# Performance work log

Hardware: AMD Instinct MI355X
Metric: run time of the kernel (lower is better)

The kernel has to match this reference:

```python
import jax, jax.numpy as jnp
import numpy as np

N = 65536          # nodes
E = 1048576        # edges (avg degree 16)
K = 5              # B-spline kernel size per dim (dim=3 -> 125 kernels)
F_IN, F_OUT = 1, 32
GRID = 32          # first sparse_voxel_max_pool: size = 1/32 -> 32^3 voxels
NUM_VOX = GRID ** 3

# enumerate the 2^3 corners of the degree-1 B-spline support
_BITS = np.array([[(b >> d) & 1 for d in range(3)] for b in range(8)], dtype=np.int32)  # [8,3]
_STRIDES = np.array([1, K, K * K], dtype=np.int32)  # kernel index strides per dim


def setup_inputs() -> dict:
    key = jax.random.key(0)
    ks = jax.random.split(key, 7)
    x = jax.random.normal(ks[0], (N, F_IN), dtype=jnp.float32)
    edge_index = jax.random.randint(ks[1], (2, E), 0, N, dtype=jnp.int32)
    pseudo = jax.random.uniform(ks[2], (E, 3), dtype=jnp.float32)   # edge pseudo-coords in [0,1]^3
    pos = jax.random.uniform(ks[3], (N, 3), dtype=jnp.float32)      # node positions in [0,1]^3
    W = jax.random.normal(ks[4], (K ** 3, F_IN, F_OUT), dtype=jnp.float32) * 0.1
    W_root = jax.random.normal(ks[5], (F_IN, F_OUT), dtype=jnp.float32) * 0.1
    bias = jax.random.normal(ks[6], (F_OUT,), dtype=jnp.float32) * 0.1
    return {"x": x, "edge_index": edge_index, "pseudo": pseudo, "pos": pos,
            "W": W, "W_root": W_root, "bias": bias}


def spline_basis(pseudo):
    """Degree-1 open B-spline basis. Returns (weights [E,8], kernel_idx [E,8])."""
    v = pseudo * (K - 1)                                   # [E,3] in [0, K-1]
    i0 = jnp.clip(jnp.floor(v), 0, K - 2)                  # lower knot per dim
    f = v - i0                                             # fractional part
    i0 = i0.astype(jnp.int32)
    bits = jnp.asarray(_BITS)                              # [8,3]
    idx = i0[:, None, :] + bits[None]                      # [E,8,3]
    w = jnp.where(bits[None].astype(bool), f[:, None, :], 1.0 - f[:, None, :])
    B = w.prod(axis=-1)                                    # [E,8]
    kidx = (idx * jnp.asarray(_STRIDES)).sum(axis=-1)      # [E,8] in [0,125)
    return B, kidx


def spline_conv(x, edge_index, pseudo, W, W_root, bias):
    src, dst = edge_index[0], edge_index[1]
    B, kidx = spline_basis(pseudo)                         # [E,8], [E,8]
    xj = x[src]                                            # [E,F_IN] edge-wise gather
    Wg = W[kidx]                                           # [E,8,F_IN,F_OUT]
    msg = jnp.einsum('es,ef,esfo->eo', B, xj, Wg)          # basis-weighted messages [E,F_OUT]
    agg = jax.ops.segment_sum(msg, dst, num_segments=N)    # scatter-add
    deg = jax.ops.segment_sum(jnp.ones((E,), jnp.float32), dst, num_segments=N)
    out = agg / jnp.clip(deg, 1.0)[:, None] + x @ W_root + bias  # mean aggr + root + bias
    return out


def reference(x, edge_index, pseudo, pos, W, W_root, bias):
    h = jax.nn.elu(spline_conv(x, edge_index, pseudo, W, W_root, bias))  # [N,32]
    # sparse voxel max pooling: hash positions to a 32^3 grid, scatter-max features
    vid = jnp.clip(jnp.floor(pos * GRID), 0, GRID - 1).astype(jnp.int32)  # [N,3]
    vidx = vid[:, 0] + GRID * vid[:, 1] + GRID * GRID * vid[:, 2]         # [N]
    pooled = jax.ops.segment_max(h, vidx, num_segments=NUM_VOX)           # [32768,32]
    pooled = jnp.where(jnp.isfinite(pooled), pooled, 0.0)                 # empty voxels -> 0
    return pooled
```

## Files before the change

### kernel.cpp

```cpp
#include <hip/hip_runtime.h>
#include <math.h>

#define F_OUT     32
#define GRID_DIM  32
#define NUM_VOX   (GRID_DIM * GRID_DIM * GRID_DIM)

#define NGRP  256
#define GNPB  256
#define HNPB  128
#define SEB   2048
#define EPT   4
#define BCAP  4480
#define SCS   132
#define DEGS  125
#define CSTR  32

__device__ __forceinline__ unsigned int enc_f32(float f) {
    unsigned int u = __float_as_uint(f);
    return (u & 0x80000000u) ? ~u : (u | 0x80000000u);
}
__device__ __forceinline__ float dec_f32(unsigned int e) {
    return (e & 0x80000000u) ? __uint_as_float(e ^ 0x80000000u)
                             : __uint_as_float(~e);
}

__global__ __launch_bounds__(512) void scatter_kernel(
    const int*   __restrict__ src,
    const int*   __restrict__ dst,
    const float* __restrict__ x,
    const float* __restrict__ pseudo,
    float4* __restrict__ payload,
    unsigned int* __restrict__ cursor,
    int E)
{
    __shared__ unsigned int sHist[NGRP];
    __shared__ unsigned int sStart[NGRP];
    __shared__ unsigned int sGBase[NGRP];
    __shared__ unsigned int sTotal;
    __shared__ unsigned short sGid[SEB];
    __shared__ __align__(16) float4 sPay[SEB];

    const int t  = threadIdx.x;
    const int e0 = blockIdx.x * SEB;

    if (t < NGRP) sHist[t] = 0;
    __syncthreads();

    unsigned short dloc[EPT];
    float4 pay[EPT];
    bool   val[EPT];
    #pragma unroll
    for (int i = 0; i < EPT; ++i) {
        int e = e0 + i * 512 + t;
        val[i] = (e < E);
        if (val[i]) {
            int d = dst[e];
            int s = src[e];
            float p0 = pseudo[3 * e], p1 = pseudo[3 * e + 1], p2 = pseudo[3 * e + 2];
            float xj = x[s];
            unsigned int q2 = (unsigned int)(p2 * 65535.0f + 0.5f) & 0xFFFFu;
            pay[i]  = make_float4(p0, p1, xj,
                        __uint_as_float(q2 | ((unsigned int)(d & 255) << 16)));
            dloc[i] = (unsigned short)d;
            atomicAdd(&sHist[(d >> 8) & 255], 1u);
        } else dloc[i] = 0;
    }
    __syncthreads();

    if (t < 64) {
        unsigned int c0 = sHist[4*t], c1 = sHist[4*t+1], c2 = sHist[4*t+2], c3 = sHist[4*t+3];
        unsigned int loc = c0 + c1 + c2 + c3;
        unsigned int incl = loc;
        #pragma unroll
        for (int d = 1; d < 64; d <<= 1) {
            unsigned int v = __shfl_up(incl, d, 64);
            if (t >= d) incl += v;
        }
        unsigned int excl = incl - loc;
        sStart[4*t]   = excl;
        sStart[4*t+1] = excl + c0;
        sStart[4*t+2] = excl + c0 + c1;
        sStart[4*t+3] = excl + c0 + c1 + c2;
        if (t == 63) sTotal = incl;
    }
    __syncthreads();

    if (t < NGRP) {
        unsigned int c = sHist[t];
        sGBase[t] = c ? atomicAdd(&cursor[(size_t)t * CSTR], c) : 0u;
        sHist[t]  = sStart[t];
    }
    __syncthreads();

    #pragma unroll
    for (int i = 0; i < EPT; ++i) {
        if (val[i]) {
            unsigned int g = ((unsigned int)dloc[i] >> 8) & 255u;
            unsigned int slot = atomicAdd(&sHist[g], 1u);
            sPay[slot] = pay[i];
            sGid[slot] = (unsigned short)g;
        }
    }
    __syncthreads();

    const unsigned int total = sTotal;
    for (unsigned int i = t; i < total; i += 512) {
        unsigned int g   = sGid[i];
        unsigned int idx = sGBase[g] + (i - sStart[g]);
        if (idx < BCAP)
            payload[(size_t)g * BCAP + idx] = sPay[i];
    }
}

__device__ __forceinline__ void process_edge(float4 r, float* sC, int half)
{
    unsigned int w = __float_as_uint(r.w);
    int rel8 = (int)((w >> 16) & 255u);
    if ((rel8 >> 7) != half) return;

    float xj = r.z;
    float p2 = (float)(w & 0xFFFFu) * (1.0f / 65535.0f);

    float v0 = r.x * 4.0f, v1 = r.y * 4.0f, v2 = p2 * 4.0f;
    float i0 = fminf(fmaxf(floorf(v0), 0.0f), 3.0f);
    float i1 = fminf(fmaxf(floorf(v1), 0.0f), 3.0f);
    float i2 = fminf(fmaxf(floorf(v2), 0.0f), 3.0f);
    float f0 = v0 - i0, f1 = v1 - i1, f2 = v2 - i2;
    float g0 = 1.0f - f0, g1 = 1.0f - f1, g2 = 1.0f - f2;
    int k = (int)i0 + 5 * (int)i1 + 25 * (int)i2;

    float w00 = g0 * g1, w10 = f0 * g1, w01 = g0 * f1, w11 = f0 * f1;
    float a2 = xj * g2, b2 = xj * f2;
    float* row = sC + (rel8 & 127) * SCS;
    atomicAdd(row + k +  0, w00 * a2);
    atomicAdd(row + k +  1, w10 * a2);
    atomicAdd(row + k +  5, w01 * a2);
    atomicAdd(row + k +  6, w11 * a2);
    atomicAdd(row + k + 25, w00 * b2);
    atomicAdd(row + k + 26, w10 * b2);
    atomicAdd(row + k + 30, w01 * b2);
    atomicAdd(row + k + 31, w11 * b2);
    atomicAdd(row + DEGS, 1.0f);
}

__global__ __launch_bounds__(256) void owner_kernel(
    const float4* __restrict__ payload,
    const unsigned int* __restrict__ cursor,
    const float* __restrict__ W,
    const float* __restrict__ x,
    const float* __restrict__ W_root,
    const float* __restrict__ bias,
    const float* __restrict__ pos,
    unsigned int* __restrict__ pooled,
    int Nn)
{
    __shared__ __align__(16) float sC[HNPB * SCS];

    const int t    = threadIdx.x;
    const int g    = blockIdx.x >> 1;
    const int half = blockIdx.x & 1;

    for (int i = t; i < HNPB * SCS / 4; i += 256)
        ((float4*)sC)[i] = make_float4(0.f, 0.f, 0.f, 0.f);

    int cnt = (int)cursor[(size_t)g * CSTR];
    if (cnt > BCAP) cnt = BCAP;
    const float4* slab = payload + (size_t)g * BCAP;
    __syncthreads();

    {
        int i = t;
        if (i < cnt) {
            float4 r = slab[i];
            for (i += 256; i < cnt; i += 256) {
                float4 rn = slab[i];
                process_edge(r, sC, half);
                r = rn;
            }
            process_edge(r, sC, half);
        }
    }
    __syncthreads();

    const int nl = t & 31;
    const int cg = t >> 5;
    const float4 wr = *(const float4*)(W_root + cg * 4);
    const float4 bs = *(const float4*)(bias + cg * 4);

    #pragma unroll
    for (int tile = 0; tile < 4; ++tile) {
        const int node = tile * 32 + nl;
        const float* crow = sC + node * SCS;
        float4 acc = make_float4(0.f, 0.f, 0.f, 0.f);
        #pragma unroll 8
        for (int k4 = 0; k4 < 31; ++k4) {
            float4 r = *(const float4*)&crow[k4 * 4];
            const float* wp = W + (k4 * 4) * F_OUT + cg * 4;
            float4 w0 = *(const float4*)(wp);
            float4 w1 = *(const float4*)(wp + F_OUT);
            float4 w2 = *(const float4*)(wp + 2 * F_OUT);
            float4 w3 = *(const float4*)(wp + 3 * F_OUT);
            acc.x += r.x * w0.x + r.y * w1.x + r.z * w2.x + r.w * w3.x;
            acc.y += r.x * w0.y + r.y * w1.y + r.z * w2.y + r.w * w3.y;
            acc.z += r.x * w0.z + r.y * w1.z + r.z * w2.z + r.w * w3.z;
            acc.w += r.x * w0.w + r.y * w1.w + r.z * w2.w + r.w * w3.w;
        }
        {
            float r = crow[124];
            const float* wp = W + 124 * F_OUT + cg * 4;
            acc.x += r * wp[0]; acc.y += r * wp[1];
            acc.z += r * wp[2]; acc.w += r * wp[3];
        }
        float dg = fmaxf(crow[DEGS], 1.0f);
        int   n  = g * GNPB + half * HNPB + node;
        float xn = (n < Nn) ? x[n] : 0.0f;
        __syncthreads();
        if (n < Nn) {
            float h;
            h = acc.x / dg + xn * wr.x + bs.x; h = h > 0.f ? h : expm1f(h); sC[node * SCS + cg * 4 + 0] = h;
            h = acc.y / dg + xn * wr.y + bs.y; h = h > 0.f ? h : expm1f(h); sC[node * SCS + cg * 4 + 1] = h;
            h = acc.z / dg + xn * wr.z + bs.z; h = h > 0.f ? h : expm1f(h); sC[node * SCS + cg * 4 + 2] = h;
            h = acc.w / dg + xn * wr.w + bs.w; h = h > 0.f ? h : expm1f(h); sC[node * SCS + cg * 4 + 3] = h;
        }
    }
    __syncthreads();

    for (int item = t; item < HNPB * F_OUT; item += 256) {
        int nr = item >> 5, o = item & 31;
        int nn = g * GNPB + half * HNPB + nr;
        if (nn >= Nn) continue;
        int vx = min(max((int)floorf(pos[3 * nn + 0] * (float)GRID_DIM), 0), GRID_DIM - 1);
        int vy = min(max((int)floorf(pos[3 * nn + 1] * (float)GRID_DIM), 0), GRID_DIM - 1);
        int vz = min(max((int)floorf(pos[3 * nn + 2] * (float)GRID_DIM), 0), GRID_DIM - 1);
        int vidx = vx + GRID_DIM * vy + GRID_DIM * GRID_DIM * vz;
        atomicMax(&pooled[(size_t)vidx * F_OUT + o], enc_f32(sC[nr * SCS + o]));
    }
}

__global__ __launch_bounds__(256) void finalize_kernel(
    const unsigned int* pooled,
    float* out, int M)
{
    int i = blockIdx.x * blockDim.x + threadIdx.x;
    if (i >= M) return;
    unsigned int u = pooled[i];
    out[i] = (u == 0u) ? 0.0f : dec_f32(u);
}

extern "C" void kernel_launch(void* const* d_in, const int* in_sizes, int n_in,
                              void* d_out, int out_size, void* d_ws, size_t ws_size,
                              hipStream_t stream) {
    const float* x       = (const float*)d_in[0];
    const int*   ei      = (const int*)  d_in[1];
    const float* pseudo  = (const float*)d_in[2];
    const float* pos     = (const float*)d_in[3];
    const float* W       = (const float*)d_in[4];
    const float* W_root  = (const float*)d_in[5];
    const float* bias    = (const float*)d_in[6];

    const int E    = in_sizes[1] / 2;
    const int Nn   = in_sizes[0];
    const int nSB  = (E + SEB - 1) / SEB;
    const int nb   = 2 * ((Nn + GNPB - 1) / GNPB);

    float4*       payload = (float4*)d_ws;
    unsigned int* cursor  = (unsigned int*)((char*)d_ws + (size_t)NGRP * BCAP * sizeof(float4));

    unsigned int* pooled = (unsigned int*)d_out;
    const int M = (out_size < NUM_VOX * F_OUT) ? out_size : NUM_VOX * F_OUT;

    hipMemsetAsync(cursor, 0, (size_t)NGRP * CSTR * sizeof(unsigned int), stream);
    hipMemsetAsync(d_out, 0, (size_t)M * sizeof(float), stream);

    scatter_kernel<<<nSB, 512, 0, stream>>>(ei, ei + E, x, pseudo, payload, cursor, E);
    owner_kernel<<<nb, 256, 0, stream>>>(payload, cursor, W, x, W_root, bias, pos,
                                         pooled, Nn);
    finalize_kernel<<<(M + 255) / 256, 256, 0, stream>>>(pooled, (float*)d_out, M);
}
```

Before: 179.4 us.

## Bucket edges into 512 groups of 128 nodes so owner blocks read only their own edges

The scatter pass now buckets edges by destination into 512 groups of 128 nodes instead of 256 groups of 256. Each owner block handles one group with 512 threads and no longer skips the half of its slab that belongs to the other half-block. This removes the duplicated payload reads and rejection checks, since each edge is read once instead of twice. In exchange the scatter histogram grows and slab capacity per group shrinks to 2560, which risks overflow and silently dropped edges if a group gets more edges than the cap.

```diff
diff --git a/kernel.cpp b/kernel.cpp
--- a/kernel.cpp
+++ b/kernel.cpp
@@ -5,12 +5,11 @@
 #define GRID_DIM  32
 #define NUM_VOX   (GRID_DIM * GRID_DIM * GRID_DIM)
 
-#define NGRP  256
-#define GNPB  256
+#define NGRP  512
 #define HNPB  128
 #define SEB   2048
 #define EPT   4
-#define BCAP  4480
+#define BCAP  2560
 #define SCS   132
 #define DEGS  125
 #define CSTR  32
@@ -43,7 +42,7 @@
     const int t  = threadIdx.x;
     const int e0 = blockIdx.x * SEB;
 
-    if (t < NGRP) sHist[t] = 0;
+    sHist[t] = 0;
     __syncthreads();
 
     unsigned short dloc[EPT];
@@ -60,32 +59,31 @@
             float xj = x[s];
             unsigned int q2 = (unsigned int)(p2 * 65535.0f + 0.5f) & 0xFFFFu;
             pay[i]  = make_float4(p0, p1, xj,
-                        __uint_as_float(q2 | ((unsigned int)(d & 255) << 16)));
+                        __uint_as_float(q2 | ((unsigned int)(d & 127) << 16)));
             dloc[i] = (unsigned short)d;
-            atomicAdd(&sHist[(d >> 8) & 255], 1u);
+            atomicAdd(&sHist[(d >> 7) & (NGRP - 1)], 1u);
         } else dloc[i] = 0;
     }
     __syncthreads();
 
     if (t < 64) {
-        unsigned int c0 = sHist[4*t], c1 = sHist[4*t+1], c2 = sHist[4*t+2], c3 = sHist[4*t+3];
-        unsigned int loc = c0 + c1 + c2 + c3;
+        unsigned int c[8], loc = 0;
+        #pragma unroll
+        for (int j = 0; j < 8; ++j) { c[j] = sHist[8 * t + j]; loc += c[j]; }
         unsigned int incl = loc;
         #pragma unroll
         for (int d = 1; d < 64; d <<= 1) {
             unsigned int v = __shfl_up(incl, d, 64);
             if (t >= d) incl += v;
         }
-        unsigned int excl = incl - loc;
-        sStart[4*t]   = excl;
-        sStart[4*t+1] = excl + c0;
-        sStart[4*t+2] = excl + c0 + c1;
-        sStart[4*t+3] = excl + c0 + c1 + c2;
-        if (t == 63) sTotal = incl;
-    }
-    __syncthreads();
-
-    if (t < NGRP) {
+        unsigned int run = incl - loc;
+        #pragma unroll
+        for (int j = 0; j < 8; ++j) { sStart[8 * t + j] = run; run += c[j]; }
+        if (t == 63) sTotal = run;
+    }
+    __syncthreads();
+
+    {
         unsigned int c = sHist[t];
         sGBase[t] = c ? atomicAdd(&cursor[(size_t)t * CSTR], c) : 0u;
         sHist[t]  = sStart[t];
@@ -95,7 +93,7 @@
     #pragma unroll
     for (int i = 0; i < EPT; ++i) {
         if (val[i]) {
-            unsigned int g = ((unsigned int)dloc[i] >> 8) & 255u;
+            unsigned int g = ((unsigned int)dloc[i] >> 7) & (NGRP - 1);
             unsigned int slot = atomicAdd(&sHist[g], 1u);
             sPay[slot] = pay[i];
             sGid[slot] = (unsigned short)g;
@@ -112,11 +110,10 @@
     }
 }
 
-__device__ __forceinline__ void process_edge(float4 r, float* sC, int half)
+__device__ __forceinline__ void process_edge(float4 r, float* sC)
 {
     unsigned int w = __float_as_uint(r.w);
-    int rel8 = (int)((w >> 16) & 255u);
-    if ((rel8 >> 7) != half) return;
+    int rel = (int)((w >> 16) & 127u);
 
     float xj = r.z;
     float p2 = (float)(w & 0xFFFFu) * (1.0f / 65535.0f);
@@ -131,7 +128,7 @@
 
     float w00 = g0 * g1, w10 = f0 * g1, w01 = g0 * f1, w11 = f0 * f1;
     float a2 = xj * g2, b2 = xj * f2;
-    float* row = sC + (rel8 & 127) * SCS;
+    float* row = sC + rel * SCS;
     atomicAdd(row + k +  0, w00 * a2);
     atomicAdd(row + k +  1, w10 * a2);
     atomicAdd(row + k +  5, w01 * a2);
@@ -143,7 +140,7 @@
     atomicAdd(row + DEGS, 1.0f);
 }
 
-__global__ __launch_bounds__(256) void owner_kernel(
+__global__ __launch_bounds__(512) void owner_kernel(
     const float4* __restrict__ payload,
     const unsigned int* __restrict__ cursor,
     const float* __restrict__ W,
@@ -156,11 +153,10 @@
 {
     __shared__ __align__(16) float sC[HNPB * SCS];
 
-    const int t    = threadIdx.x;
-    const int g    = blockIdx.x >> 1;
-    const int half = blockIdx.x & 1;
-
-    for (int i = t; i < HNPB * SCS / 4; i += 256)
+    const int t = threadIdx.x;
+    const int g = blockIdx.x;
+
+    for (int i = t; i < HNPB * SCS / 4; i += 512)
         ((float4*)sC)[i] = make_float4(0.f, 0.f, 0.f, 0.f);
 
     int cnt = (int)cursor[(size_t)g * CSTR];
@@ -172,24 +168,24 @@
         int i = t;
         if (i < cnt) {
             float4 r = slab[i];
-            for (i += 256; i < cnt; i += 256) {
+            for (i += 512; i < cnt; i += 512) {
                 float4 rn = slab[i];
-                process_edge(r, sC, half);
+                process_edge(r, sC);
                 r = rn;
             }
-            process_edge(r, sC, half);
-        }
-    }
-    __syncthreads();
-
-    const int nl = t & 31;
-    const int cg = t >> 5;
+            process_edge(r, sC);
+        }
+    }
+    __syncthreads();
+
+    const int nl = t & 63;
+    const int cg = t >> 6;
     const float4 wr = *(const float4*)(W_root + cg * 4);
     const float4 bs = *(const float4*)(bias + cg * 4);
 
     #pragma unroll
-    for (int tile = 0; tile < 4; ++tile) {
-        const int node = tile * 32 + nl;
+    for (int tile = 0; tile < 2; ++tile) {
+        const int node = tile * 64 + nl;
         const float* crow = sC + node * SCS;
         float4 acc = make_float4(0.f, 0.f, 0.f, 0.f);
         #pragma unroll 8
@@ -212,7 +208,7 @@
             acc.z += r * wp[2]; acc.w += r * wp[3];
         }
         float dg = fmaxf(crow[DEGS], 1.0f);
-        int   n  = g * GNPB + half * HNPB + node;
+        int   n  = g * HNPB + node;
         float xn = (n < Nn) ? x[n] : 0.0f;
         __syncthreads();
         if (n < Nn) {
@@ -225,9 +221,9 @@
     }
     __syncthreads();
 
-    for (int item = t; item < HNPB * F_OUT; item += 256) {
+    for (int item = t; item < HNPB * F_OUT; item += 512) {
         int nr = item >> 5, o = item & 31;
-        int nn = g * GNPB + half * HNPB + nr;
+        int nn = g * HNPB + nr;
         if (nn >= Nn) continue;
         int vx = min(max((int)floorf(pos[3 * nn + 0] * (float)GRID_DIM), 0), GRID_DIM - 1);
         int vy = min(max((int)floorf(pos[3 * nn + 1] * (float)GRID_DIM), 0), GRID_DIM - 1);
@@ -258,10 +254,10 @@
     const float* W_root  = (const float*)d_in[5];
     const float* bias    = (const float*)d_in[6];
 
-    const int E    = in_sizes[1] / 2;
-    const int Nn   = in_sizes[0];
-    const int nSB  = (E + SEB - 1) / SEB;
-    const int nb   = 2 * ((Nn + GNPB - 1) / GNPB);
+    const int E   = in_sizes[1] / 2;
+    const int Nn  = in_sizes[0];
+    const int nSB = (E + SEB - 1) / SEB;
+    const int nb  = (Nn + HNPB - 1) / HNPB;
 
     float4*       payload = (float4*)d_ws;
     unsigned int* cursor  = (unsigned int*)((char*)d_ws + (size_t)NGRP * BCAP * sizeof(float4));
@@ -273,7 +269,7 @@
     hipMemsetAsync(d_out, 0, (size_t)M * sizeof(float), stream);
 
     scatter_kernel<<<nSB, 512, 0, stream>>>(ei, ei + E, x, pseudo, payload, cursor, E);
-    owner_kernel<<<nb, 256, 0, stream>>>(payload, cursor, W, x, W_root, bias, pos,
+    owner_kernel<<<nb, 512, 0, stream>>>(payload, cursor, W, x, W_root, bias, pos,
                                          pooled, Nn);
     finalize_kernel<<<(M + 255) / 256, 256, 0, stream>>>(pooled, (float*)d_out, M);
 }
```

New measurement: 182.4 us. Within noise of the previous version (+1.7%).
